# Kernel optimization log

Measured on AMD Instinct MI355X. Metric: run time of the kernel, lower is better.

## Reference

```python
import jax, jax.numpy as jnp
import numpy as np
import math

B, T, E = 2, 2048, 1024
H = 16
D = E // H  # head_dim = 64

def setup_inputs() -> dict:
    key = jax.random.key(0)
    k1, k2, k3, k4, k5 = jax.random.split(key, 5)
    s = 0.02
    return {
        "x": jax.random.normal(k1, (B, T, E), dtype=jnp.float32),
        "W_attn": jax.random.normal(k2, (E, 3 * E), dtype=jnp.float32) * s,
        "b_attn": jax.random.normal(k3, (3 * E,), dtype=jnp.float32) * s,
        "W_proj": jax.random.normal(k4, (E, E), dtype=jnp.float32) * s,
        "b_proj": jax.random.normal(k5, (E,), dtype=jnp.float32) * s,
    }

def reference(x, W_attn, b_attn, W_proj, b_proj):
    Bx, Tx, Ex = x.shape
    qkv = x @ W_attn + b_attn                      # [B,T,3E]
    q, k, v = jnp.split(qkv, 3, axis=2)
    # [B,T,E] -> [B,H,T,D]
    def heads(t):
        return t.reshape(Bx, Tx, H, D).transpose(0, 2, 1, 3)
    q, k, v = heads(q), heads(k), heads(v)
    scores = jnp.einsum('bhqd,bhkd->bhqk', q, k) / math.sqrt(D)
    causal = jnp.tril(jnp.ones((Tx, Tx), dtype=bool))
    scores = jnp.where(causal, scores, -jnp.inf)
    attn = jax.nn.softmax(scores, axis=-1)
    out = jnp.einsum('bhqk,bhkd->bhqd', attn, v)   # [B,H,T,D]
    out = out.transpose(0, 2, 1, 3).reshape(Bx, Tx, Ex)
    return out @ W_proj + b_proj
```

## Files before the change

kernel.cpp:

```cpp
#include <hip/hip_runtime.h>


typedef unsigned short u16;
typedef __bf16 bf8 __attribute__((ext_vector_type(8)));
typedef float f32x4 __attribute__((ext_vector_type(4)));

struct __align__(8) u16x4s { u16 v[4]; };

__device__ __forceinline__ u16 f2b(float f) {
    return __builtin_bit_cast(u16, (__bf16)f);
}

__device__ __forceinline__ f32x4 mfma16(bf8 a, bf8 b, f32x4 c) {
    return __builtin_amdgcn_mfma_f32_16x16x32_bf16(a, b, c, 0, 0, 0);
}

__device__ __forceinline__ float fexp2(float x) {
    return __builtin_amdgcn_exp2f(x);
}

__device__ __forceinline__ void gload_lds16(const u16* g, u16* l) {
    __builtin_amdgcn_global_load_lds(
        (__attribute__((address_space(1))) void*)(g),
        (__attribute__((address_space(3))) void*)(l), 16, 0, 0);
}

__global__ __launch_bounds__(256) void k_prep(const float* __restrict__ x,
                                              const float* __restrict__ Wa,
                                              const float* __restrict__ Wp,
                                              u16* __restrict__ Xb,
                                              u16* __restrict__ WtA,
                                              u16* __restrict__ WtP) {
    __shared__ float tile[64][65];
    int id = blockIdx.x, t = threadIdx.x;
    if (id < 4096) {
        int i = id * 256 + t;
        float4 v = ((const float4*)x)[i];
        ushort4 o;
        o.x = f2b(v.x); o.y = f2b(v.y); o.z = f2b(v.z); o.w = f2b(v.w);
        ((ushort4*)Xb)[i] = o;
        return;
    }
    const float* in; u16* out; int N, j;
    if (id < 4864) { j = id - 4096; in = Wa; out = WtA; N = 3072; }
    else           { j = id - 4864; in = Wp; out = WtP; N = 1024; }
    int k0 = (j & 15) * 64, n0 = (j >> 4) * 64;
    int c = t & 63, r0 = t >> 6;
#pragma unroll
    for (int i = 0; i < 16; ++i) {
        int r = r0 + i * 4;
        tile[r][c] = in[(size_t)(k0 + r) * N + n0 + c];
    }
    __syncthreads();
#pragma unroll
    for (int i = 0; i < 16; ++i) {
        int r = r0 + i * 4;
        out[(size_t)(n0 + r) * 1024 + k0 + c] = f2b(tile[c][r]);
    }
}

#define GEMM_STAGE(GA0, GA1, GB0, GB1, K, B)                                   \
    do {                                                                       \
        gload_lds16(GA0 + (K), As[B] + tid * 8);                               \
        gload_lds16(GA1 + (K), As[B] + (256 + tid) * 8);                       \
        gload_lds16(GB0 + (K), Bs[B] + tid * 8);                               \
        gload_lds16(GB1 + (K), Bs[B] + (256 + tid) * 8);                       \
    } while (0)

#define GEMM_CORE(Aptr, Bptr)                                                  \
    int tid = threadIdx.x;                                                     \
    int w = tid >> 6, lane = tid & 63, l16 = lane & 15, quad = lane >> 4;      \
    int m0 = blockIdx.x * 128, n0 = blockIdx.y * 128;                          \
    int wr = (w >> 1) * 64, wc = (w & 1) * 64;                                 \
    __shared__ u16 As[2][128 * 32];                                            \
    __shared__ u16 Bs[2][128 * 32];                                            \
    f32x4 acc[4][4];                                                           \
    _Pragma("unroll") for (int mi = 0; mi < 4; ++mi)                           \
        _Pragma("unroll") for (int ni = 0; ni < 4; ++ni)                       \
            _Pragma("unroll") for (int r = 0; r < 4; ++r) acc[mi][ni][r] = 0.f;\
    int srow0 = tid >> 2, srow1 = 64 + srow0;                                  \
    int slc = ((tid & 3) ^ ((tid >> 3) & 3)) * 8;      \
    const u16* gA0 = Aptr + (size_t)(m0 + srow0) * 1024 + slc;                 \
    const u16* gA1 = Aptr + (size_t)(m0 + srow1) * 1024 + slc;                 \
    const u16* gB0 = Bptr + (size_t)(n0 + srow0) * 1024 + slc;                 \
    const u16* gB1 = Bptr + (size_t)(n0 + srow1) * 1024 + slc;                 \
    int cq = (quad ^ ((l16 >> 1) & 3)) * 8;               \
    GEMM_STAGE(gA0, gA1, gB0, gB1, 0, 0);                                      \
    for (int it = 0; it < 32; ++it) {                                          \
        int pb = it & 1;                                                       \
        __syncthreads();                           \
        bf8 af[4], bf[4];                                                      \
        _Pragma("unroll") for (int mi = 0; mi < 4; ++mi)                       \
            af[mi] = *(const bf8*)(As[pb] + (wr + mi * 16 + l16) * 32 + cq);   \
        _Pragma("unroll") for (int ni = 0; ni < 4; ++ni)                       \
            bf[ni] = *(const bf8*)(Bs[pb] + (wc + ni * 16 + l16) * 32 + cq);   \
        if (it < 31) GEMM_STAGE(gA0, gA1, gB0, gB1, (it + 1) * 32, pb ^ 1);    \
        _Pragma("unroll") for (int mi = 0; mi < 4; ++mi)                       \
            _Pragma("unroll") for (int ni = 0; ni < 4; ++ni)                   \
                acc[mi][ni] = mfma16(af[mi], bf[ni], acc[mi][ni]);             \
    }

__global__ __launch_bounds__(256, 3) void k_qkv(const u16* __restrict__ Xb,
                                                const u16* __restrict__ WtA,
                                                const float* __restrict__ ba,
                                                u16* __restrict__ Qb,
                                                u16* __restrict__ Kb,
                                                u16* __restrict__ Vtb) {
    GEMM_CORE(Xb, WtA)
    int sel = n0 >> 10;
    u16* dst = sel == 0 ? Qb : (sel == 1 ? Kb : Vtb);
    const float qs = 0.18033688011112042f;
#pragma unroll
    for (int ni = 0; ni < 4; ++ni) {
        int n = n0 + wc + ni * 16 + l16;
        float bias = ba[n];
        int h = (n & 1023) >> 6;
        int d = n & 63;
#pragma unroll
        for (int mi = 0; mi < 4; ++mi)
#pragma unroll
            for (int r = 0; r < 4; ++r) {
                int m = m0 + wr + mi * 16 + quad * 4 + r;
                int bb = m >> 11, tt = m & 2047;
                float v = acc[mi][ni][r] + bias;
                size_t hb = (size_t)(bb * 16 + h);
                if (sel == 2)
                    dst[hb * 131072 + (size_t)(tt >> 6) * 4096 + d * 64 + (tt & 63)] = f2b(v);
                else
                    dst[(hb * 2048 + tt) * 64 + d] =
                        f2b(sel == 0 ? v * qs : v);
            }
    }
}

__global__ __launch_bounds__(256, 3) void k_proj(const u16* __restrict__ AO,
                                                 const u16* __restrict__ WtP,
                                                 const float* __restrict__ bp,
                                                 float* __restrict__ out) {
    GEMM_CORE(AO, WtP)
#pragma unroll
    for (int ni = 0; ni < 4; ++ni) {
        int n = n0 + wc + ni * 16 + l16;
        float bias = bp[n];
#pragma unroll
        for (int mi = 0; mi < 4; ++mi)
#pragma unroll
            for (int r = 0; r < 4; ++r) {
                int m = m0 + wr + mi * 16 + quad * 4 + r;
                out[(size_t)m * 1024 + n] = acc[mi][ni][r] + bias;
            }
    }
}


#define STAGE(KT, B) do {                                                     \
    int ci0_ = tid, ci1_ = 256 + tid;                                         \
    const u16* kt_ = Kh + (size_t)(KT) * 4096;                                \
    gload_lds16(kt_ + (ci0_ >> 3) * 64 +                                      \
                (((ci0_ & 7) ^ ((ci0_ >> 5) & 7)) * 8), Ks[B] + ci0_ * 8);    \
    gload_lds16(kt_ + (ci1_ >> 3) * 64 +                                      \
                (((ci1_ & 7) ^ ((ci1_ >> 5) & 7)) * 8), Ks[B] + ci1_ * 8);    \
    const u16* vt_ = Vh + (size_t)(KT) * 4096;                                \
    gload_lds16(vt_ + (ci0_ >> 3) * 64 +                                      \
                (((ci0_ & 7) ^ ((ci0_ >> 3) & 7)) * 8), Vs[B] + ci0_ * 8);    \
    gload_lds16(vt_ + (ci1_ >> 3) * 64 +                                      \
                (((ci1_ & 7) ^ ((ci1_ >> 3) & 7)) * 8), Vs[B] + ci1_ * 8);    \
} while (0)

#define QK_SOFT(KT, KF, QF0, QF1, LI, QROW, KTM, PBUF) do {                   \
    int kb_ = (KT) * 64;                                                      \
    bool diag_ = ((KT) == (KTM));                                             \
    f32x4 s_acc[4];                                                           \
    _Pragma("unroll") for (int s = 0; s < 4; ++s)                             \
        _Pragma("unroll") for (int r = 0; r < 4; ++r) s_acc[s][r] = 0.f;      \
    _Pragma("unroll") for (int sub = 0; sub < 4; ++sub) {                     \
        s_acc[sub] = mfma16(QF0, KF[sub][0], s_acc[sub]);                     \
        s_acc[sub] = mfma16(QF1, KF[sub][1], s_acc[sub]);                     \
    }                                                                         \
    _Pragma("unroll") for (int r = 0; r < 4; ++r) {                           \
        float p[4];                                                           \
        if (diag_) {                                                          \
            int qg_ = (QROW) + quad * 4 + r;                                  \
            _Pragma("unroll") for (int sub = 0; sub < 4; ++sub) {             \
                int key_ = kb_ + 4 * l16 + sub;                               \
                p[sub] = fexp2(key_ <= qg_ ? s_acc[sub][r] : -1e30f);         \
            }                                                                 \
        } else {                                                              \
            _Pragma("unroll") for (int sub = 0; sub < 4; ++sub)               \
                p[sub] = fexp2(s_acc[sub][r]);                                \
        }                                                                     \
        LI[r] += (p[0] + p[1]) + (p[2] + p[3]);                               \
        u16x4s pk_;                                                           \
        _Pragma("unroll") for (int sub = 0; sub < 4; ++sub)                   \
            pk_.v[sub] = f2b(p[sub]);                                         \
        int prow_ = quad * 4 + r;                                             \
        *(u16x4s*)&PBUF[prow_][(((l16 >> 1) ^ (prow_ & 7)) << 3) +            \
                               ((l16 & 1) << 2)] = pk_;     \
    }                                                                         \
} while (0)

#define PV_ACC(VF, PBUF, OACC) do {                                           \
    int xp_ = l16 & 7;                                                        \
    bf8 pf0 = *(const bf8*)&PBUF[l16][(quad ^ xp_) << 3];                     \
    bf8 pf1 = *(const bf8*)&PBUF[l16][((4 + quad) ^ xp_) << 3];               \
    _Pragma("unroll") for (int dt = 0; dt < 4; ++dt) {                        \
        OACC[dt] = mfma16(pf0, VF[dt][0], OACC[dt]);                          \
        OACC[dt] = mfma16(pf1, VF[dt][1], OACC[dt]);                          \
    }                                                                         \
} while (0)

__global__ __launch_bounds__(256, 2) void k_attn(const u16* __restrict__ Qb,
                                                 const u16* __restrict__ Kb,
                                                 const u16* __restrict__ Vtb,
                                                 u16* __restrict__ AO) {
    int id = blockIdx.x;
    int bh = (id & 7) * 4 + ((id >> 3) & 3);
    int t  = 15 - (id >> 5);
    int tid = threadIdx.x;
    int w = tid >> 6, lane = tid & 63, l16 = lane & 15, quad = lane >> 4;

    const u16* Qh = Qb  + (size_t)bh * 2048 * 64;
    const u16* Kh = Kb  + (size_t)bh * 2048 * 64;
    const u16* Vh = Vtb + (size_t)bh * 131072;

    int qrA = t * 64 + w * 16;
    int qrB = qrA + 1024;
    int ktmaxA = t, ktmaxB = t + 16;

    __shared__ u16 Ks[2][64 * 64];
    __shared__ u16 Vs[2][64 * 64];
    __shared__ u16 P[4][2][16][64];

    bf8 qfA0 = *(const bf8*)(Qh + (size_t)(qrA + l16) * 64 + quad * 8);
    bf8 qfA1 = *(const bf8*)(Qh + (size_t)(qrA + l16) * 64 + 32 + quad * 8);
    bf8 qfB0 = *(const bf8*)(Qh + (size_t)(qrB + l16) * 64 + quad * 8);
    bf8 qfB1 = *(const bf8*)(Qh + (size_t)(qrB + l16) * 64 + 32 + quad * 8);

    float l_iA[4] = {0.f, 0.f, 0.f, 0.f};
    float l_iB[4] = {0.f, 0.f, 0.f, 0.f};
    f32x4 o_accA[4], o_accB[4];
#pragma unroll
    for (int dt = 0; dt < 4; ++dt)
#pragma unroll
        for (int r = 0; r < 4; ++r) { o_accA[dt][r] = 0.f; o_accB[dt][r] = 0.f; }

    int xsw = (l16 & 7) * 8;

    STAGE(0, 0);
    for (int kt = 0; kt <= ktmaxB; ++kt) {
        int pb = kt & 1;
        __syncthreads();

        bf8 kf[4][2], vf[4][2];
        const u16* kb_ = Ks[pb];
        const u16* vb_ = Vs[pb];
#pragma unroll
        for (int sub = 0; sub < 4; ++sub)
#pragma unroll
            for (int ks = 0; ks < 2; ++ks)
                kf[sub][ks] = *(const bf8*)(kb_ + (4 * l16 + sub) * 64 +
                                            (((ks * 32 + quad * 8)) ^ xsw));
#pragma unroll
        for (int dt = 0; dt < 4; ++dt)
#pragma unroll
            for (int ks = 0; ks < 2; ++ks)
                vf[dt][ks] = *(const bf8*)(vb_ + (dt * 16 + l16) * 64 +
                                           (((ks * 32 + quad * 8)) ^ xsw));

        if (kt < ktmaxB) STAGE(kt + 1, pb ^ 1);

        bool aAct = (kt <= ktmaxA);
        if (aAct) QK_SOFT(kt, kf, qfA0, qfA1, l_iA, qrA, ktmaxA, P[w][0]);
        QK_SOFT(kt, kf, qfB0, qfB1, l_iB, qrB, ktmaxB, P[w][1]);
        asm volatile("s_waitcnt lgkmcnt(0)" ::: "memory");
        __builtin_amdgcn_sched_barrier(0);
        if (aAct) PV_ACC(vf, P[w][0], o_accA);
        PV_ACC(vf, P[w][1], o_accB);
    }

    float linvA[4], linvB[4];
#pragma unroll
    for (int r = 0; r < 4; ++r) {
        float la = l_iA[r], lb = l_iB[r];
        la += __shfl_xor(la, 1, 64); lb += __shfl_xor(lb, 1, 64);
        la += __shfl_xor(la, 2, 64); lb += __shfl_xor(lb, 2, 64);
        la += __shfl_xor(la, 4, 64); lb += __shfl_xor(lb, 4, 64);
        la += __shfl_xor(la, 8, 64); lb += __shfl_xor(lb, 8, 64);
        linvA[r] = __builtin_amdgcn_rcpf(la);
        linvB[r] = __builtin_amdgcn_rcpf(lb);
    }

    int b = bh >> 4, h = bh & 15;
#pragma unroll
    for (int dt = 0; dt < 4; ++dt)
#pragma unroll
        for (int r = 0; r < 4; ++r) {
            int off = quad * 4 + r;
            size_t rowA = (size_t)b * 2048 + qrA + off;
            size_t rowB = (size_t)b * 2048 + qrB + off;
            AO[rowA * 1024 + h * 64 + dt * 16 + l16] = f2b(o_accA[dt][r] * linvA[r]);
            AO[rowB * 1024 + h * 64 + dt * 16 + l16] = f2b(o_accB[dt][r] * linvB[r]);
        }
}

extern "C" void kernel_launch(void* const* d_in, const int* in_sizes, int n_in,
                              void* d_out, int out_size, void* d_ws, size_t ws_size,
                              hipStream_t stream) {
    const float* x  = (const float*)d_in[0];
    const float* Wa = (const float*)d_in[1];
    const float* ba = (const float*)d_in[2];
    const float* Wp = (const float*)d_in[3];
    const float* bp = (const float*)d_in[4];
    float* out = (float*)d_out;

    char* ws = (char*)d_ws;
    const size_t MB = 1024 * 1024;
    u16* Xb  = (u16*)(ws);
    u16* WtA = (u16*)(ws + 8  * MB);
    u16* WtP = (u16*)(ws + 14 * MB);
    u16* Qb  = (u16*)(ws + 16 * MB);
    u16* Kb  = (u16*)(ws + 24 * MB);
    u16* Vtb = (u16*)(ws + 32 * MB);
    u16* AO  = Xb;

    k_prep<<<dim3(5120),    dim3(256), 0, stream>>>(x, Wa, Wp, Xb, WtA, WtP);
    k_qkv <<<dim3(32, 24),  dim3(256), 0, stream>>>(Xb, WtA, ba, Qb, Kb, Vtb);
    k_attn<<<dim3(512),     dim3(256), 0, stream>>>(Qb, Kb, Vtb, AO);
    k_proj<<<dim3(32, 8),   dim3(256), 0, stream>>>(AO, WtP, bp, out);
}
```

Before: 173.4 us.

## Restructure attention into single-wave blocks with four interleaved query tiles

```diff
diff --git a/kernel.cpp b/kernel.cpp
--- a/kernel.cpp
+++ b/kernel.cpp
@@ -153,18 +153,19 @@
 }
 
 
-#define STAGE(KT, B) do {                                                     \
-    int ci0_ = tid, ci1_ = 256 + tid;                                         \
+#define STAGE1(KT, B) do {                                                    \
     const u16* kt_ = Kh + (size_t)(KT) * 4096;                                \
-    gload_lds16(kt_ + (ci0_ >> 3) * 64 +                                      \
-                (((ci0_ & 7) ^ ((ci0_ >> 5) & 7)) * 8), Ks[B] + ci0_ * 8);    \
-    gload_lds16(kt_ + (ci1_ >> 3) * 64 +                                      \
-                (((ci1_ & 7) ^ ((ci1_ >> 5) & 7)) * 8), Ks[B] + ci1_ * 8);    \
     const u16* vt_ = Vh + (size_t)(KT) * 4096;                                \
-    gload_lds16(vt_ + (ci0_ >> 3) * 64 +                                      \
-                (((ci0_ & 7) ^ ((ci0_ >> 3) & 7)) * 8), Vs[B] + ci0_ * 8);    \
-    gload_lds16(vt_ + (ci1_ >> 3) * 64 +                                      \
-                (((ci1_ & 7) ^ ((ci1_ >> 3) & 7)) * 8), Vs[B] + ci1_ * 8);    \
+    _Pragma("unroll") for (int i_ = 0; i_ < 8; ++i_) {                        \
+        int ci_ = i_ * 64 + lane;                                             \
+        gload_lds16(kt_ + (ci_ >> 3) * 64 +                                   \
+                    (((ci_ & 7) ^ ((ci_ >> 5) & 7)) * 8), Ks[B] + ci_ * 8);   \
+    }                                                                         \
+    _Pragma("unroll") for (int i_ = 0; i_ < 8; ++i_) {                        \
+        int ci_ = i_ * 64 + lane;                                             \
+        gload_lds16(vt_ + (ci_ >> 3) * 64 +                                   \
+                    (((ci_ & 7) ^ ((ci_ >> 3) & 7)) * 8), Vs[B] + ci_ * 8);   \
+    }                                                                         \
 } while (0)
 
 #define QK_SOFT(KT, KF, QF0, QF1, LI, QROW, KTM, PBUF) do {                   \
@@ -209,47 +210,78 @@
     }                                                                         \
 } while (0)
 
-__global__ __launch_bounds__(256, 2) void k_attn(const u16* __restrict__ Qb,
-                                                 const u16* __restrict__ Kb,
-                                                 const u16* __restrict__ Vtb,
-                                                 u16* __restrict__ AO) {
+#define LREDUCE(LI, LINV) do {                                                \
+    _Pragma("unroll") for (int r = 0; r < 4; ++r) {                           \
+        float s_ = LI[r];                                                     \
+        s_ += __shfl_xor(s_, 1, 64); s_ += __shfl_xor(s_, 2, 64);             \
+        s_ += __shfl_xor(s_, 4, 64); s_ += __shfl_xor(s_, 8, 64);             \
+        LINV[r] = __builtin_amdgcn_rcpf(s_);                                  \
+    }                                                                         \
+} while (0)
+
+#define STORE_O(OA, LINV, QR) do {                                            \
+    _Pragma("unroll") for (int dt = 0; dt < 4; ++dt)                          \
+        _Pragma("unroll") for (int r = 0; r < 4; ++r) {                       \
+            int off_ = quad * 4 + r;                                          \
+            size_t row_ = (size_t)b * 2048 + (QR) + off_;                     \
+            AO[row_ * 1024 + h * 64 + dt * 16 + l16] =                        \
+                f2b(OA[dt][r] * LINV[r]);                                     \
+        }                                                                     \
+} while (0)
+
+__global__ __launch_bounds__(64, 1) void k_attn(const u16* __restrict__ Qb,
+                                                const u16* __restrict__ Kb,
+                                                const u16* __restrict__ Vtb,
+                                                u16* __restrict__ AO) {
     int id = blockIdx.x;
     int bh = (id & 7) * 4 + ((id >> 3) & 3);
-    int t  = 15 - (id >> 5);
-    int tid = threadIdx.x;
-    int w = tid >> 6, lane = tid & 63, l16 = lane & 15, quad = lane >> 4;
-
-    const u16* Qh = Qb  + (size_t)bh * 2048 * 64;
-    const u16* Kh = Kb  + (size_t)bh * 2048 * 64;
+    int t  = id >> 5;
+    int lane = threadIdx.x & 63, l16 = lane & 15, quad = lane >> 4;
+
+    const u16* Qh = Qb  + (size_t)bh * 131072;
+    const u16* Kh = Kb  + (size_t)bh * 131072;
     const u16* Vh = Vtb + (size_t)bh * 131072;
 
-    int qrA = t * 64 + w * 16;
-    int qrB = qrA + 1024;
-    int ktmaxA = t, ktmaxB = t + 16;
-
-    __shared__ u16 Ks[2][64 * 64];
-    __shared__ u16 Vs[2][64 * 64];
-    __shared__ u16 P[4][2][16][64];
-
-    bf8 qfA0 = *(const bf8*)(Qh + (size_t)(qrA + l16) * 64 + quad * 8);
-    bf8 qfA1 = *(const bf8*)(Qh + (size_t)(qrA + l16) * 64 + 32 + quad * 8);
-    bf8 qfB0 = *(const bf8*)(Qh + (size_t)(qrB + l16) * 64 + quad * 8);
-    bf8 qfB1 = *(const bf8*)(Qh + (size_t)(qrB + l16) * 64 + 32 + quad * 8);
-
-    float l_iA[4] = {0.f, 0.f, 0.f, 0.f};
-    float l_iB[4] = {0.f, 0.f, 0.f, 0.f};
-    f32x4 o_accA[4], o_accB[4];
+    __shared__ u16 Ks[2][4096];
+    __shared__ u16 Vs[2][4096];
+    __shared__ u16 P[2][16][64];
+
+    int qr0 = t * 16, qr1 = qr0 + 512, qr2 = qr0 + 1024, qr3 = qr0 + 1536;
+    int ktm0 = t >> 2, ktm1 = ktm0 + 8, ktm2 = ktm0 + 16, ktm3 = ktm0 + 24;
+
+    bf8 qf0[4], qf1[4];
+#pragma unroll
+    for (int j = 0; j < 4; ++j) {
+        int qr = t * 16 + j * 512;
+        qf0[j] = *(const bf8*)(Qh + (size_t)(qr + l16) * 64 + quad * 8);
+        qf1[j] = *(const bf8*)(Qh + (size_t)(qr + l16) * 64 + 32 + quad * 8);
+    }
+
+    float li0[4], li1[4], li2[4], li3[4];
+    f32x4 oa0[4], oa1[4], oa2[4], oa3[4];
+#pragma unroll
+    for (int r = 0; r < 4; ++r) { li0[r] = li1[r] = li2[r] = li3[r] = 0.f; }
 #pragma unroll
     for (int dt = 0; dt < 4; ++dt)
 #pragma unroll
-        for (int r = 0; r < 4; ++r) { o_accA[dt][r] = 0.f; o_accB[dt][r] = 0.f; }
+        for (int r = 0; r < 4; ++r) {
+            oa0[dt][r] = 0.f; oa1[dt][r] = 0.f;
+            oa2[dt][r] = 0.f; oa3[dt][r] = 0.f;
+        }
 
     int xsw = (l16 & 7) * 8;
 
-    STAGE(0, 0);
-    for (int kt = 0; kt <= ktmaxB; ++kt) {
+    STAGE1(0, 0);
+    int nkt = ktm3 + 1;
+    for (int kt = 0; kt < nkt; ++kt) {
         int pb = kt & 1;
-        __syncthreads();
+        if (kt + 1 < nkt) {
+            STAGE1(kt + 1, pb ^ 1);
+            asm volatile("s_waitcnt vmcnt(16)" ::: "memory");
+        } else {
+            asm volatile("s_waitcnt vmcnt(0)" ::: "memory");
+        }
+        __builtin_amdgcn_sched_barrier(0);
 
         bf8 kf[4][2], vf[4][2];
         const u16* kb_ = Ks[pb];
@@ -267,40 +299,31 @@
                 vf[dt][ks] = *(const bf8*)(vb_ + (dt * 16 + l16) * 64 +
                                            (((ks * 32 + quad * 8)) ^ xsw));
 
-        if (kt < ktmaxB) STAGE(kt + 1, pb ^ 1);
-
-        bool aAct = (kt <= ktmaxA);
-        if (aAct) QK_SOFT(kt, kf, qfA0, qfA1, l_iA, qrA, ktmaxA, P[w][0]);
-        QK_SOFT(kt, kf, qfB0, qfB1, l_iB, qrB, ktmaxB, P[w][1]);
+        bool a0 = (kt <= ktm0), a1 = (kt <= ktm1), a2 = (kt <= ktm2);
+
+        if (a0) QK_SOFT(kt, kf, qf0[0], qf1[0], li0, qr0, ktm0, P[0]);
+        if (a1) QK_SOFT(kt, kf, qf0[1], qf1[1], li1, qr1, ktm1, P[1]);
         asm volatile("s_waitcnt lgkmcnt(0)" ::: "memory");
         __builtin_amdgcn_sched_barrier(0);
-        if (aAct) PV_ACC(vf, P[w][0], o_accA);
-        PV_ACC(vf, P[w][1], o_accB);
-    }
-
-    float linvA[4], linvB[4];
-#pragma unroll
-    for (int r = 0; r < 4; ++r) {
-        float la = l_iA[r], lb = l_iB[r];
-        la += __shfl_xor(la, 1, 64); lb += __shfl_xor(lb, 1, 64);
-        la += __shfl_xor(la, 2, 64); lb += __shfl_xor(lb, 2, 64);
-        la += __shfl_xor(la, 4, 64); lb += __shfl_xor(lb, 4, 64);
-        la += __shfl_xor(la, 8, 64); lb += __shfl_xor(lb, 8, 64);
-        linvA[r] = __builtin_amdgcn_rcpf(la);
-        linvB[r] = __builtin_amdgcn_rcpf(lb);
-    }
+        if (a0) PV_ACC(vf, P[0], oa0);
+        if (a1) PV_ACC(vf, P[1], oa1);
+
+        if (a2) QK_SOFT(kt, kf, qf0[2], qf1[2], li2, qr2, ktm2, P[0]);
+        QK_SOFT(kt, kf, qf0[3], qf1[3], li3, qr3, ktm3, P[1]);
+        asm volatile("s_waitcnt lgkmcnt(0)" ::: "memory");
+        __builtin_amdgcn_sched_barrier(0);
+        if (a2) PV_ACC(vf, P[0], oa2);
+        PV_ACC(vf, P[1], oa3);
+    }
+
+    float lv0[4], lv1[4], lv2[4], lv3[4];
+    LREDUCE(li0, lv0); LREDUCE(li1, lv1); LREDUCE(li2, lv2); LREDUCE(li3, lv3);
 
     int b = bh >> 4, h = bh & 15;
-#pragma unroll
-    for (int dt = 0; dt < 4; ++dt)
-#pragma unroll
-        for (int r = 0; r < 4; ++r) {
-            int off = quad * 4 + r;
-            size_t rowA = (size_t)b * 2048 + qrA + off;
-            size_t rowB = (size_t)b * 2048 + qrB + off;
-            AO[rowA * 1024 + h * 64 + dt * 16 + l16] = f2b(o_accA[dt][r] * linvA[r]);
-            AO[rowB * 1024 + h * 64 + dt * 16 + l16] = f2b(o_accB[dt][r] * linvB[r]);
-        }
+    STORE_O(oa0, lv0, qr0);
+    STORE_O(oa1, lv1, qr1);
+    STORE_O(oa2, lv2, qr2);
+    STORE_O(oa3, lv3, qr3);
 }
 
 extern "C" void kernel_launch(void* const* d_in, const int* in_sizes, int n_in,
@@ -325,6 +348,6 @@
 
     k_prep<<<dim3(5120),    dim3(256), 0, stream>>>(x, Wa, Wp, Xb, WtA, WtP);
     k_qkv <<<dim3(32, 24),  dim3(256), 0, stream>>>(Xb, WtA, ba, Qb, Kb, Vtb);
-    k_attn<<<dim3(512),     dim3(256), 0, stream>>>(Qb, Kb, Vtb, AO);
+    k_attn<<<dim3(1024),    dim3(64),  0, stream>>>(Qb, Kb, Vtb, AO);
     k_proj<<<dim3(32, 8),   dim3(256), 0, stream>>>(AO, WtP, bp, out);
 }
```

Result: slower. 196.7 us (+13.4%).

## Rewrite attention inner loop with 32x32 MFMA and register-resident P

Applied to the files above, without the earlier changes.

```diff
diff --git a/kernel.cpp b/kernel.cpp
--- a/kernel.cpp
+++ b/kernel.cpp
@@ -2,17 +2,26 @@
 
 
 typedef unsigned short u16;
+typedef unsigned int u32;
 typedef __bf16 bf8 __attribute__((ext_vector_type(8)));
 typedef float f32x4 __attribute__((ext_vector_type(4)));
-
-struct __align__(8) u16x4s { u16 v[4]; };
+typedef float f32x16 __attribute__((ext_vector_type(16)));
+typedef u32 u32x4v __attribute__((ext_vector_type(4)));
 
 __device__ __forceinline__ u16 f2b(float f) {
     return __builtin_bit_cast(u16, (__bf16)f);
 }
 
+__device__ __forceinline__ u32 pk2(float lo, float hi) {
+    return (u32)f2b(lo) | ((u32)f2b(hi) << 16);
+}
+
 __device__ __forceinline__ f32x4 mfma16(bf8 a, bf8 b, f32x4 c) {
     return __builtin_amdgcn_mfma_f32_16x16x32_bf16(a, b, c, 0, 0, 0);
+}
+
+__device__ __forceinline__ f32x16 mfma32(bf8 a, bf8 b, f32x16 c) {
+    return __builtin_amdgcn_mfma_f32_32x32x16_bf16(a, b, c, 0, 0, 0);
 }
 
 __device__ __forceinline__ float fexp2(float x) {
@@ -157,56 +166,31 @@
     int ci0_ = tid, ci1_ = 256 + tid;                                         \
     const u16* kt_ = Kh + (size_t)(KT) * 4096;                                \
     gload_lds16(kt_ + (ci0_ >> 3) * 64 +                                      \
-                (((ci0_ & 7) ^ ((ci0_ >> 5) & 7)) * 8), Ks[B] + ci0_ * 8);    \
+                (((ci0_ & 7) ^ ((ci0_ >> 5) & 7)) * 8), KV[B][0] + ci0_ * 8); \
     gload_lds16(kt_ + (ci1_ >> 3) * 64 +                                      \
-                (((ci1_ & 7) ^ ((ci1_ >> 5) & 7)) * 8), Ks[B] + ci1_ * 8);    \
+                (((ci1_ & 7) ^ ((ci1_ >> 5) & 7)) * 8), KV[B][0] + ci1_ * 8); \
     const u16* vt_ = Vh + (size_t)(KT) * 4096;                                \
     gload_lds16(vt_ + (ci0_ >> 3) * 64 +                                      \
-                (((ci0_ & 7) ^ ((ci0_ >> 3) & 7)) * 8), Vs[B] + ci0_ * 8);    \
+                (((ci0_ & 7) ^ ((ci0_ >> 3) & 7)) * 8), KV[B][1] + ci0_ * 8); \
     gload_lds16(vt_ + (ci1_ >> 3) * 64 +                                      \
-                (((ci1_ & 7) ^ ((ci1_ >> 3) & 7)) * 8), Vs[B] + ci1_ * 8);    \
+                (((ci1_ & 7) ^ ((ci1_ >> 3) & 7)) * 8), KV[B][1] + ci1_ * 8); \
 } while (0)
 
-#define QK_SOFT(KT, KF, QF0, QF1, LI, QROW, KTM, PBUF) do {                   \
-    int kb_ = (KT) * 64;                                                      \
-    bool diag_ = ((KT) == (KTM));                                             \
-    f32x4 s_acc[4];                                                           \
-    _Pragma("unroll") for (int s = 0; s < 4; ++s)                             \
-        _Pragma("unroll") for (int r = 0; r < 4; ++r) s_acc[s][r] = 0.f;      \
-    _Pragma("unroll") for (int sub = 0; sub < 4; ++sub) {                     \
-        s_acc[sub] = mfma16(QF0, KF[sub][0], s_acc[sub]);                     \
-        s_acc[sub] = mfma16(QF1, KF[sub][1], s_acc[sub]);                     \
-    }                                                                         \
-    _Pragma("unroll") for (int r = 0; r < 4; ++r) {                           \
-        float p[4];                                                           \
-        if (diag_) {                                                          \
-            int qg_ = (QROW) + quad * 4 + r;                                  \
-            _Pragma("unroll") for (int sub = 0; sub < 4; ++sub) {             \
-                int key_ = kb_ + 4 * l16 + sub;                               \
-                p[sub] = fexp2(key_ <= qg_ ? s_acc[sub][r] : -1e30f);         \
-            }                                                                 \
-        } else {                                                              \
-            _Pragma("unroll") for (int sub = 0; sub < 4; ++sub)               \
-                p[sub] = fexp2(s_acc[sub][r]);                                \
-        }                                                                     \
-        LI[r] += (p[0] + p[1]) + (p[2] + p[3]);                               \
-        u16x4s pk_;                                                           \
-        _Pragma("unroll") for (int sub = 0; sub < 4; ++sub)                   \
-            pk_.v[sub] = f2b(p[sub]);                                         \
-        int prow_ = quad * 4 + r;                                             \
-        *(u16x4s*)&PBUF[prow_][(((l16 >> 1) ^ (prow_ & 7)) << 3) +            \
-                               ((l16 & 1) << 2)] = pk_;     \
-    }                                                                         \
+#define PVSTEP(SG, BFR) do {                                                  \
+    bf8 va_ = *(const bf8*)(vb_ + l31 * 64 +                                  \
+                            (((2 * (SG) + h) ^ vswz) * 8));                   \
+    bf8 vc_ = *(const bf8*)(vb_ + (32 + l31) * 64 +                           \
+                            (((2 * (SG) + h) ^ vswz) * 8));                   \
+    bf8 pf_ = __builtin_bit_cast(bf8, BFR);                                   \
+    oT0 = mfma32(va_, pf_, oT0);                                              \
+    oT1 = mfma32(vc_, pf_, oT1);                                              \
 } while (0)
 
-#define PV_ACC(VF, PBUF, OACC) do {                                           \
-    int xp_ = l16 & 7;                                                        \
-    bf8 pf0 = *(const bf8*)&PBUF[l16][(quad ^ xp_) << 3];                     \
-    bf8 pf1 = *(const bf8*)&PBUF[l16][((4 + quad) ^ xp_) << 3];               \
-    _Pragma("unroll") for (int dt = 0; dt < 4; ++dt) {                        \
-        OACC[dt] = mfma16(pf0, VF[dt][0], OACC[dt]);                          \
-        OACC[dt] = mfma16(pf1, VF[dt][1], OACC[dt]);                          \
-    }                                                                         \
+#define BFRAGS(PK, PP, B0, B1) do {                                           \
+    B0[0] = h ? PP[2] : PK[0]; B0[1] = h ? PP[3] : PK[1];                     \
+    B0[2] = h ? PK[2] : PP[0]; B0[3] = h ? PK[3] : PP[1];                     \
+    B1[0] = h ? PP[6] : PK[4]; B1[1] = h ? PP[7] : PK[5];                     \
+    B1[2] = h ? PK[6] : PP[4]; B1[3] = h ? PK[7] : PP[5];                     \
 } while (0)
 
 __global__ __launch_bounds__(256, 2) void k_attn(const u16* __restrict__ Qb,
@@ -217,90 +201,138 @@
     int bh = (id & 7) * 4 + ((id >> 3) & 3);
     int t  = 15 - (id >> 5);
     int tid = threadIdx.x;
-    int w = tid >> 6, lane = tid & 63, l16 = lane & 15, quad = lane >> 4;
-
-    const u16* Qh = Qb  + (size_t)bh * 2048 * 64;
-    const u16* Kh = Kb  + (size_t)bh * 2048 * 64;
+    int w = tid >> 6, lane = tid & 63, l31 = lane & 31, h = lane >> 5;
+
+    const u16* Qh = Qb  + (size_t)bh * 131072;
+    const u16* Kh = Kb  + (size_t)bh * 131072;
     const u16* Vh = Vtb + (size_t)bh * 131072;
 
-    int qrA = t * 64 + w * 16;
-    int qrB = qrA + 1024;
-    int ktmaxA = t, ktmaxB = t + 16;
-
-    __shared__ u16 Ks[2][64 * 64];
-    __shared__ u16 Vs[2][64 * 64];
-    __shared__ u16 P[4][2][16][64];
-
-    bf8 qfA0 = *(const bf8*)(Qh + (size_t)(qrA + l16) * 64 + quad * 8);
-    bf8 qfA1 = *(const bf8*)(Qh + (size_t)(qrA + l16) * 64 + 32 + quad * 8);
-    bf8 qfB0 = *(const bf8*)(Qh + (size_t)(qrB + l16) * 64 + quad * 8);
-    bf8 qfB1 = *(const bf8*)(Qh + (size_t)(qrB + l16) * 64 + 32 + quad * 8);
-
-    float l_iA[4] = {0.f, 0.f, 0.f, 0.f};
-    float l_iB[4] = {0.f, 0.f, 0.f, 0.f};
-    f32x4 o_accA[4], o_accB[4];
-#pragma unroll
-    for (int dt = 0; dt < 4; ++dt)
-#pragma unroll
-        for (int r = 0; r < 4; ++r) { o_accA[dt][r] = 0.f; o_accB[dt][r] = 0.f; }
-
-    int xsw = (l16 & 7) * 8;
+    __shared__ u16 KV[2][2][4096];
+
+    int tq = t + 16 * w;
+    int qr = tq * 32;
+    int ktmax = tq >> 1;
+    int nkt = ((t + 48) >> 1) + 1;
+
+    bf8 qf[4];
+#pragma unroll
+    for (int s = 0; s < 4; ++s)
+        qf[s] = *(const bf8*)(Qh + (size_t)(qr + l31) * 64 + s * 16 + h * 8);
+
+    float l_acc = 0.f;
+    f32x16 oT0, oT1;
+#pragma unroll
+    for (int r = 0; r < 16; ++r) { oT0[r] = 0.f; oT1[r] = 0.f; }
+
+    int kswz = (l31 >> 2) & 7;
+    int vswz = l31 & 7;
 
     STAGE(0, 0);
-    for (int kt = 0; kt <= ktmaxB; ++kt) {
+    for (int kt = 0; kt < nkt; ++kt) {
         int pb = kt & 1;
         __syncthreads();
-
-        bf8 kf[4][2], vf[4][2];
-        const u16* kb_ = Ks[pb];
-        const u16* vb_ = Vs[pb];
-#pragma unroll
-        for (int sub = 0; sub < 4; ++sub)
-#pragma unroll
-            for (int ks = 0; ks < 2; ++ks)
-                kf[sub][ks] = *(const bf8*)(kb_ + (4 * l16 + sub) * 64 +
-                                            (((ks * 32 + quad * 8)) ^ xsw));
-#pragma unroll
-        for (int dt = 0; dt < 4; ++dt)
-#pragma unroll
-            for (int ks = 0; ks < 2; ++ks)
-                vf[dt][ks] = *(const bf8*)(vb_ + (dt * 16 + l16) * 64 +
-                                           (((ks * 32 + quad * 8)) ^ xsw));
-
-        if (kt < ktmaxB) STAGE(kt + 1, pb ^ 1);
-
-        bool aAct = (kt <= ktmaxA);
-        if (aAct) QK_SOFT(kt, kf, qfA0, qfA1, l_iA, qrA, ktmaxA, P[w][0]);
-        QK_SOFT(kt, kf, qfB0, qfB1, l_iB, qrB, ktmaxB, P[w][1]);
-        asm volatile("s_waitcnt lgkmcnt(0)" ::: "memory");
-        __builtin_amdgcn_sched_barrier(0);
-        if (aAct) PV_ACC(vf, P[w][0], o_accA);
-        PV_ACC(vf, P[w][1], o_accB);
-    }
-
-    float linvA[4], linvB[4];
-#pragma unroll
-    for (int r = 0; r < 4; ++r) {
-        float la = l_iA[r], lb = l_iB[r];
-        la += __shfl_xor(la, 1, 64); lb += __shfl_xor(lb, 1, 64);
-        la += __shfl_xor(la, 2, 64); lb += __shfl_xor(lb, 2, 64);
-        la += __shfl_xor(la, 4, 64); lb += __shfl_xor(lb, 4, 64);
-        la += __shfl_xor(la, 8, 64); lb += __shfl_xor(lb, 8, 64);
-        linvA[r] = __builtin_amdgcn_rcpf(la);
-        linvB[r] = __builtin_amdgcn_rcpf(lb);
-    }
-
-    int b = bh >> 4, h = bh & 15;
-#pragma unroll
-    for (int dt = 0; dt < 4; ++dt)
-#pragma unroll
-        for (int r = 0; r < 4; ++r) {
-            int off = quad * 4 + r;
-            size_t rowA = (size_t)b * 2048 + qrA + off;
-            size_t rowB = (size_t)b * 2048 + qrB + off;
-            AO[rowA * 1024 + h * 64 + dt * 16 + l16] = f2b(o_accA[dt][r] * linvA[r]);
-            AO[rowB * 1024 + h * 64 + dt * 16 + l16] = f2b(o_accB[dt][r] * linvB[r]);
+        if (kt + 1 < nkt) STAGE(kt + 1, pb ^ 1);
+
+        if (kt <= ktmax) {
+            const u16* kb_ = KV[pb][0];
+            const u16* vb_ = KV[pb][1];
+            bool diag = (kt == ktmax);
+            bool doK1 = !(diag && ((tq & 1) == 0));
+
+            f32x16 sT0, sT1;
+#pragma unroll
+            for (int r = 0; r < 16; ++r) { sT0[r] = 0.f; sT1[r] = 0.f; }
+#pragma unroll
+            for (int s = 0; s < 4; ++s) {
+                bf8 kf = *(const bf8*)(kb_ + l31 * 64 +
+                                       (((2 * s + h) ^ kswz) * 8));
+                sT0 = mfma32(kf, qf[s], sT0);
+            }
+            if (doK1) {
+#pragma unroll
+                for (int s = 0; s < 4; ++s) {
+                    bf8 kf = *(const bf8*)(kb_ + (32 + l31) * 64 +
+                                           (((2 * s + h) ^ kswz) * 8));
+                    sT1 = mfma32(kf, qf[s], sT1);
+                }
+            }
+
+            int kb0 = kt * 64, qg = qr + l31;
+            if (diag) {
+#pragma unroll
+                for (int r = 0; r < 16; ++r) {
+                    int krow = kb0 + (r & 3) + 8 * (r >> 2) + 4 * h;
+                    sT0[r] = fexp2(krow <= qg ? sT0[r] : -1e30f);
+                    l_acc += sT0[r];
+                }
+                if (doK1) {
+#pragma unroll
+                    for (int r = 0; r < 16; ++r) {
+                        int krow = kb0 + 32 + (r & 3) + 8 * (r >> 2) + 4 * h;
+                        sT1[r] = fexp2(krow <= qg ? sT1[r] : -1e30f);
+                        l_acc += sT1[r];
+                    }
+                }
+            } else {
+#pragma unroll
+                for (int r = 0; r < 16; ++r) {
+                    sT0[r] = fexp2(sT0[r]); l_acc += sT0[r];
+                }
+#pragma unroll
+                for (int r = 0; r < 16; ++r) {
+                    sT1[r] = fexp2(sT1[r]); l_acc += sT1[r];
+                }
+            }
+
+            u32 pka[8], ppa[8];
+#pragma unroll
+            for (int j = 0; j < 8; ++j)
+                pka[j] = pk2(sT0[2 * j], sT0[2 * j + 1]);
+#pragma unroll
+            for (int j = 0; j < 8; ++j)
+                ppa[j] = __shfl_xor(pka[j], 32, 64);
+            u32x4v bf0, bf1;
+            BFRAGS(pka, ppa, bf0, bf1);
+            PVSTEP(0, bf0);
+            PVSTEP(1, bf1);
+            if (doK1) {
+                u32 pkb[8], ppb[8];
+#pragma unroll
+                for (int j = 0; j < 8; ++j)
+                    pkb[j] = pk2(sT1[2 * j], sT1[2 * j + 1]);
+#pragma unroll
+                for (int j = 0; j < 8; ++j)
+                    ppb[j] = __shfl_xor(pkb[j], 32, 64);
+                u32x4v bg0, bg1;
+                BFRAGS(pkb, ppb, bg0, bg1);
+                PVSTEP(2, bg0);
+                PVSTEP(3, bg1);
+            }
         }
+    }
+
+    __syncthreads();
+    float lsum = l_acc + __shfl_xor(l_acc, 32, 64);
+    float linv = __builtin_amdgcn_rcpf(lsum);
+
+    u32* Ot = (u32*)(&KV[0][0][0]) + w * 1152;
+#pragma unroll
+    for (int j = 0; j < 8; ++j) {
+        int col = 4 * (j >> 1) + 2 * h + (j & 1);
+        Ot[l31 * 36 + col]      = pk2(oT0[2 * j] * linv, oT0[2 * j + 1] * linv);
+        Ot[l31 * 36 + 16 + col] = pk2(oT1[2 * j] * linv, oT1[2 * j + 1] * linv);
+    }
+    asm volatile("s_waitcnt lgkmcnt(0)" ::: "memory");
+    __builtin_amdgcn_sched_barrier(0);
+
+    int q2 = lane >> 1, half = lane & 1;
+    int eb = bh >> 4, eh = bh & 15;
+    size_t row = (size_t)eb * 2048 + qr + q2;
+    const u32* src = Ot + q2 * 36 + half * 16;
+    u32* dstg = (u32*)(AO + row * 1024 + eh * 64) + half * 16;
+#pragma unroll
+    for (int c = 0; c < 4; ++c)
+        *(u32x4v*)(dstg + 4 * c) = *(const u32x4v*)(src + 4 * c);
 }
 
 extern "C" void kernel_launch(void* const* d_in, const int* in_sizes, int n_in,
```

Result: slower. 182.1 us (+5.0%).
